# Kernel optimization log

Hardware: AMD Instinct MI355X
Metric: run time of the kernel (lower is better)

## Reference

```python
import jax, jax.numpy as jnp
import numpy as np

B_IMG, T_PER, DIN = 8, 4096, 1176
D, E, BN, L, TOP_K, OUT = 1024, 8, 64, 4, 2, 4096


def setup_inputs() -> dict:
    key = jax.random.key(0)
    ks = jax.random.split(key, 16)
    s = 0.02
    inp = {
        "pixel_values": jax.random.normal(ks[0], (B_IMG * T_PER, DIN), jnp.float32),
        "image_grid_thw": jnp.tile(jnp.array([[1, 64, 64]], dtype=jnp.int64), (B_IMG, 1)),
        # in_proj (no bias)
        "w_in": jax.random.normal(ks[1], (DIN, D), jnp.float32) * s,
        # skin classifier: Linear(D,64) -> ReLU -> Linear(64,3)
        "w_sc1": jax.random.normal(ks[2], (D, 64), jnp.float32) * s,
        "b_sc1": jnp.zeros((64,), jnp.float32),
        "w_sc2": jax.random.normal(ks[3], (64, 3), jnp.float32) * s,
        "b_sc2": jnp.zeros((3,), jnp.float32),
        # per-adapter-layer routers (stacked over L)
        "w_rimg": jax.random.normal(ks[4], (L, D, E), jnp.float32) * s,
        "w_rskin": jax.random.normal(ks[5], (L, 3, E), jnp.float32) * s,
        # per-layer, per-expert MLP: Linear(D,BN) -> ReLU -> Linear(BN,D)
        "ew1": jax.random.normal(ks[6], (L, E, D, BN), jnp.float32) * s,
        "eb1": jnp.zeros((L, E, BN), jnp.float32),
        "ew2": jax.random.normal(ks[7], (L, E, BN, D), jnp.float32) * s,
        "eb2": jnp.zeros((L, E, D), jnp.float32),
        # out_proj
        "w_out": jax.random.normal(ks[8], (D, OUT), jnp.float32) * s,
        "b_out": jnp.zeros((OUT,), jnp.float32),
    }
    return inp


def _forward(pixel_values, image_grid_thw, w_in, w_sc1, b_sc1, w_sc2, b_sc2,
             w_rimg, w_rskin, ew1, eb1, ew2, eb2, w_out, b_out):
    B = image_grid_thw.shape[0]
    T = pixel_values.shape[0] // B  # equal chunk sizes (t*h*w identical per image)
    x = pixel_values.reshape(B, T, -1)

    def per_image(xc):  # xc: [T, din]
        h = xc @ w_in  # [T, D]
        g = h.mean(0)
        skin_logits = jax.nn.relu(g @ w_sc1 + b_sc1) @ w_sc2 + b_sc2  # [3]
        skin_probs = jax.nn.softmax(skin_logits)

        def layer(carry, params):
            h, aux = carry
            wri, wrs, W1, B1, W2, B2 = params
            logits = h @ wri + skin_probs @ wrs  # [T, E]
            probs = jax.nn.softmax(logits, axis=-1)
            tp, ti = jax.lax.top_k(probs, TOP_K)
            tp = tp / (tp.sum(-1, keepdims=True) + 1e-6)
            rows = jnp.arange(h.shape[0])[:, None]
            # dense per-token expert weights (0 for non-selected experts)
            wfull = jnp.zeros_like(probs).at[rows, ti].add(tp)
            mask = jnp.zeros_like(probs).at[rows, ti].add(1.0)
            h1 = jax.nn.relu(jnp.einsum('td,edb->teb', h, W1) + B1)  # [T,E,BN]
            h2 = jnp.einsum('teb,ebd->ted', h1, W2) + B2             # [T,E,D]
            moe_out = jnp.einsum('ted,te->td', h2, wfull)
            aux = aux + (probs.mean(0) * mask.mean(0)).sum() * probs.shape[-1]
            return (h + moe_out, aux), None

        (h, aux), _ = jax.lax.scan(layer, (h, jnp.zeros((), h.dtype)),
                                   (w_rimg, w_rskin, ew1, eb1, ew2, eb2))
        return h.mean(0), skin_logits, aux

    pooled, skin_logits, aux = jax.vmap(per_image)(x)
    vision_proj = pooled @ w_out + b_out
    return pooled, vision_proj, aux.sum(), skin_logits


def reference(pixel_values, image_grid_thw, w_in, w_sc1, b_sc1, w_sc2, b_sc2,
              w_rimg, w_rskin, ew1, eb1, ew2, eb2, w_out, b_out):
    return _forward(pixel_values, image_grid_thw, w_in, w_sc1, b_sc1, w_sc2, b_sc2,
                    w_rimg, w_rskin, ew1, eb1, ew2, eb2, w_out, b_out)
```

## Files before the change

kernel.cpp:

```cpp
#include <hip/hip_runtime.h>
#include <math.h>

#define TPI  4096
#define TT   32768
#define DIN  1176
#define KP   1184
#define DM   1024
#define NE   8
#define BN   64
#define NL   4
#define DOUT 4096

typedef __attribute__((ext_vector_type(4))) float floatx4;
typedef __attribute__((ext_vector_type(8))) short bf16x8;
typedef unsigned int uint;

__device__ inline short f2bf(float x) {
    unsigned u = __float_as_uint(x);
    u += 0x7fffu + ((u >> 16) & 1u);
    return (short)(u >> 16);
}
__device__ inline float bf2f(short h) {
    return __uint_as_float(((unsigned)(unsigned short)h) << 16);
}

#define GLP(p) ((const __attribute__((address_space(1))) void*)(p))
#define LDSP(p) ((__attribute__((address_space(3))) void*)(p))
#define ASYNC16(g, s) __builtin_amdgcn_global_load_lds(GLP(g), LDSP(s), 16, 0, 0)

#define OFF_H0    0ul
#define OFF_H1    67108864ul
#define OFF_XB    134217728ul
#define OFF_WBT   211812352ul
#define OFF_E1T   214237184ul
#define OFF_E2T   218431488ul
#define OFF_BTOK  222625792ul
#define OFF_BW1   222756864ul
#define OFF_BW2   222887936ul
#define OFF_T2E   223019008ul
#define OFF_T2W   223150080ul
#define OFF_WQ    223412224ul
#define OFF_Z     223416320ul
#define Z_BYTES   39232ul
#define OFF_RB    223455552ul
#define OFF_WRT   223456576ul

__global__ __launch_bounds__(256) void convx_kernel(
    const float* __restrict__ X, short* __restrict__ Xb)
{
    const long row = blockIdx.x;
    const float* src = X + row * (long)DIN;
    short* dst = Xb + row * (long)KP;
    for (int i = threadIdx.x; i < 296; i += 256) {
        short4 s;
        if (i < 294) {
            float4 v = *(const float4*)(src + i * 4);
            s.x = f2bf(v.x); s.y = f2bf(v.y); s.z = f2bf(v.z); s.w = f2bf(v.w);
        } else {
            s.x = 0; s.y = 0; s.z = 0; s.w = 0;
        }
        *(short4*)(dst + i * 4) = s;
    }
}

__global__ __launch_bounds__(256) void transp_kernel(
    const float* __restrict__ src, short* __restrict__ dst, int RS, int CS, int DK)
{
    __shared__ float tb[64][65];
    const int kt = blockIdx.x * 64, nt = blockIdx.y * 64;
    const long sb = (long)blockIdx.z * RS * CS;
    const long db = (long)blockIdx.z * CS * DK;
    const int rr = threadIdx.x >> 6, cc = threadIdx.x & 63;
#pragma unroll
    for (int i = 0; i < 16; ++i) {
        int r = i * 4 + rr;
        int k = kt + r, n = nt + cc;
        tb[r][cc] = (k < RS && n < CS) ? src[sb + (long)k * CS + n] : 0.0f;
    }
    __syncthreads();
#pragma unroll
    for (int i = 0; i < 16; ++i) {
        int r = i * 4 + rr;
        int n = nt + r, k = kt + cc;
        if (n < CS && k < DK) dst[db + (long)n * DK + k] = f2bf(tb[cc][r]);
    }
}

__global__ __launch_bounds__(256) void wrt_kernel(
    const float* __restrict__ w_rimg, short* __restrict__ wrT)
{
    const int l = blockIdx.x >> 4, e = blockIdx.x & 15;
    short* dst = wrT + ((long)l * 16 + e) * 1024;
    if (e < 8) {
        const float* src = w_rimg + (long)l * 8192 + e;
        for (int k = threadIdx.x; k < 1024; k += 256) dst[k] = f2bf(src[k * 8]);
    } else {
        for (int k = threadIdx.x; k < 1024; k += 256) dst[k] = 0;
    }
}

__global__ __launch_bounds__(256) void gemm_in_mfma(
    const short* __restrict__ Xb, const short* __restrict__ Wbt, short* __restrict__ Hb)
{
    __shared__ __align__(16) short As[128 * 32];
    __shared__ __align__(16) short Bs[128 * 32];
    const int tid = threadIdx.x;
    const int m0 = blockIdx.x * 128, n0 = blockIdx.y * 128;
    const int w = tid >> 6, lane = tid & 63;
    const int quad = lane >> 4, l15 = lane & 15;
    const int wm = (w >> 1) * 64, wn = (w & 1) * 64;

    floatx4 acc[4][4];
#pragma unroll
    for (int i = 0; i < 4; ++i)
#pragma unroll
        for (int j = 0; j < 4; ++j) acc[i][j] = 0.0f;

    const int r0 = tid >> 2, kof = (tid & 3) * 8;
    const int r1 = (tid + 256) >> 2;
    const short* a0p = Xb + (long)(m0 + r0) * KP + kof;
    const short* a1p = Xb + (long)(m0 + r1) * KP + kof;
    const short* b0p = Wbt + (long)(n0 + r0) * KP + kof;
    const short* b1p = Wbt + (long)(n0 + r1) * KP + kof;
    short* as0 = As + tid * 8;
    short* as1 = As + (tid + 256) * 8;
    short* bs0 = Bs + tid * 8;
    short* bs1 = Bs + (tid + 256) * 8;

    for (int k0 = 0; k0 < KP; k0 += 32) {
        __syncthreads();
        ASYNC16(a0p + k0, as0);
        ASYNC16(a1p + k0, as1);
        ASYNC16(b0p + k0, bs0);
        ASYNC16(b1p + k0, bs1);
        __syncthreads();
        bf16x8 af[4], bfr[4];
#pragma unroll
        for (int i = 0; i < 4; ++i)
            af[i] = *(const bf16x8*)&As[(wm + i * 16 + l15) * 32 + quad * 8];
#pragma unroll
        for (int j = 0; j < 4; ++j)
            bfr[j] = *(const bf16x8*)&Bs[(wn + j * 16 + l15) * 32 + quad * 8];
#pragma unroll
        for (int i = 0; i < 4; ++i)
#pragma unroll
            for (int j = 0; j < 4; ++j)
                acc[i][j] = __builtin_amdgcn_mfma_f32_16x16x32_bf16(af[i], bfr[j], acc[i][j], 0, 0, 0);
    }
#pragma unroll
    for (int i = 0; i < 4; ++i)
#pragma unroll
        for (int j = 0; j < 4; ++j)
#pragma unroll
            for (int r = 0; r < 4; ++r)
                Hb[(long)(m0 + wm + i * 16 + quad * 4 + r) * DM + n0 + wn + j * 16 + l15] =
                    f2bf(acc[i][j][r]);
}

__global__ __launch_bounds__(256) void colmean_kernel(
    const short* __restrict__ Hb, float* __restrict__ outp)
{
    const int col = blockIdx.x * 256 + threadIdx.x;
    const int img = blockIdx.y;
    const int t0 = blockIdx.z * 256;
    const short* p = Hb + ((long)img * TPI + t0) * DM + col;
    float s = 0.0f;
#pragma unroll 8
    for (int t = 0; t < 256; ++t) s += bf2f(p[(long)t * DM]);
    atomicAdd(&outp[img * DM + col], s * (1.0f / 4096.0f));
}

__global__ __launch_bounds__(256) void skin1_kernel(
    const float* __restrict__ g, const float* __restrict__ w_sc1,
    const float* __restrict__ b_sc1, float* __restrict__ hsg)
{
    __shared__ float red[4][64];
    const int img = blockIdx.x;
    const int part = threadIdx.x >> 6, c = threadIdx.x & 63;
    float s = 0.0f;
    for (int i = 0; i < 256; ++i) {
        int d = part * 256 + i;
        s += g[img * DM + d] * w_sc1[d * 64 + c];
    }
    red[part][c] = s;
    __syncthreads();
    if (part == 0) {
        float v = red[0][c] + red[1][c] + red[2][c] + red[3][c] + b_sc1[c];
        hsg[img * 64 + c] = fmaxf(v, 0.0f);
    }
}

__global__ __launch_bounds__(256) void skin2_kernel(
    const float* __restrict__ hsg, const float* __restrict__ w_sc2, const float* __restrict__ b_sc2,
    const float* __restrict__ w_rskin, float* __restrict__ skin_logits_out, float* __restrict__ rb)
{
    __shared__ float l3[24];
    __shared__ float sp[24];
    const int tid = threadIdx.x;
    if (tid < 24) {
        int img = tid / 3, j = tid % 3;
        float s = b_sc2[j];
        for (int c = 0; c < 64; ++c) s += hsg[img * 64 + c] * w_sc2[c * 3 + j];
        l3[tid] = s;
        skin_logits_out[tid] = s;
    }
    __syncthreads();
    if (tid < 8) {
        float v0 = l3[tid * 3], v1 = l3[tid * 3 + 1], v2 = l3[tid * 3 + 2];
        float m = fmaxf(v0, fmaxf(v1, v2));
        float e0 = expf(v0 - m), e1 = expf(v1 - m), e2 = expf(v2 - m);
        float inv = 1.0f / (e0 + e1 + e2);
        sp[tid * 3] = e0 * inv; sp[tid * 3 + 1] = e1 * inv; sp[tid * 3 + 2] = e2 * inv;
    }
    __syncthreads();
    {
        int l = tid >> 6, img = (tid >> 3) & 7, e = tid & 7;
        float s = 0.0f;
#pragma unroll
        for (int c = 0; c < 3; ++c) s += sp[img * 3 + c] * w_rskin[(l * 3 + c) * 8 + e];
        rb[tid] = s;
    }
}

__global__ __launch_bounds__(256) void router_kernel(
    const short* __restrict__ Hb, const short* __restrict__ wrT, const float* __restrict__ rb,
    uint* __restrict__ top2e, float* __restrict__ top2w, int* __restrict__ counts_pair,
    float* __restrict__ sum_probs, float* __restrict__ mask_cnt, int l)
{
    __shared__ __align__(16) short As[8 * 64 * 32];
    __shared__ float lgS[64 * 9];
    const int tid = threadIdx.x;
    const int tok0 = blockIdx.x * 64;
    const int img = tok0 >> 12;
    const int w = tid >> 6, lane = tid & 63;
    const int quad = lane >> 4, l15 = lane & 15;

    const short* rowptr = Hb + (long)(tok0 + w * 16 + (lane >> 2)) * DM + (lane & 3) * 8;
    short* sdst = As + tid * 8;
    const short* wrl = wrT + (long)l * 16 * 1024 + l15 * 1024 + quad * 8;

    floatx4 acc = 0.0f;
    for (int k0 = 0; k0 < DM; k0 += 256) {
        __syncthreads();
#pragma unroll
        for (int c = 0; c < 8; ++c) ASYNC16(rowptr + k0 + c * 32, sdst + c * 2048);
        __syncthreads();
#pragma unroll
        for (int c = 0; c < 8; ++c) {
            bf16x8 af = *(const bf16x8*)&As[c * 2048 + (w * 16 + l15) * 32 + quad * 8];
            bf16x8 bf = *(const bf16x8*)(wrl + k0 + c * 32);
            acc = __builtin_amdgcn_mfma_f32_16x16x32_bf16(af, bf, acc, 0, 0, 0);
        }
    }
    if (l15 < 8) {
#pragma unroll
        for (int r = 0; r < 4; ++r) lgS[(w * 16 + quad * 4 + r) * 9 + l15] = acc[r];
    }
    __syncthreads();

    if (tid < 64) {
        const int token = tok0 + tid;
        float p[8];
        float mx = -1e30f;
#pragma unroll
        for (int e = 0; e < 8; ++e) {
            float v = lgS[tid * 9 + e] + rb[l * 64 + img * 8 + e];
            p[e] = v; mx = fmaxf(mx, v);
        }
        float s = 0.0f;
#pragma unroll
        for (int e = 0; e < 8; ++e) { p[e] = expf(p[e] - mx); s += p[e]; }
        float inv = 1.0f / s;
#pragma unroll
        for (int e = 0; e < 8; ++e) p[e] *= inv;

        int i1 = 0; float b1v = p[0];
#pragma unroll
        for (int e = 1; e < 8; ++e) if (p[e] > b1v) { b1v = p[e]; i1 = e; }
        int i2 = -1; float b2v = -1.0f;
#pragma unroll
        for (int e = 0; e < 8; ++e) if (e != i1 && p[e] > b2v) { b2v = p[e]; i2 = e; }
        float den = b1v + b2v + 1e-6f;
        top2e[token] = (uint)i1 | ((uint)i2 << 8);
        top2w[2 * token] = b1v / den;
        top2w[2 * token + 1] = b2v / den;

        atomicAdd(&counts_pair[l * 64 + i1 * 8 + i2], 1);

        for (int slot = 0; slot < 2; ++slot) {
            int esel = slot ? i2 : i1;
#pragma unroll
            for (int e = 0; e < 8; ++e) {
                unsigned long long m = __ballot(esel == e);
                int pc = __popcll(m);
                if (pc && tid == (__ffsll(m) - 1))
                    atomicAdd(&mask_cnt[l * 64 + img * 8 + e], (float)pc);
            }
        }
#pragma unroll
        for (int e = 0; e < 8; ++e) {
            float r = p[e];
            for (int off = 32; off > 0; off >>= 1) r += __shfl_down(r, off);
            if (tid == 0) atomicAdd(&sum_probs[l * 64 + img * 8 + e], r);
        }
    }
}

__global__ __launch_bounds__(64) void wq_kernel(
    const int* __restrict__ counts_pair, int* __restrict__ wq, int* __restrict__ nworkp,
    int* __restrict__ pair_off, int l)
{
    const int p = threadIdx.x;
    int cnt = counts_pair[l * 64 + p];
    int x = cnt;
    for (int off = 1; off < 64; off <<= 1) {
        int y = __shfl_up(x, off);
        if (p >= off) x += y;
    }
    pair_off[p] = x - cnt;
    int nb = (cnt + 63) >> 6;
    int t = nb;
    for (int off = 1; off < 64; off <<= 1) {
        int y = __shfl_up(t, off);
        if (p >= off) t += y;
    }
    int start = t - nb;
    for (int i = 0; i < nb; ++i) wq[start + i] = p | ((i * 64) << 6);
    if (p == 63) nworkp[0] = t;
}

__global__ __launch_bounds__(256) void scatter_kernel(
    const uint* __restrict__ top2e, const float* __restrict__ top2w,
    const int* __restrict__ pair_off, int* __restrict__ cursors,
    int* __restrict__ btok, float* __restrict__ bw1, float* __restrict__ bw2, int l)
{
    const int t = blockIdx.x * 256 + threadIdx.x;
    const int lane = threadIdx.x & 63;
    uint pe = top2e[t];
    int p = (int)(pe & 255u) * 8 + (int)((pe >> 8) & 255u);
    float w1 = top2w[2 * t], w2 = top2w[2 * t + 1];
    int myoff = pair_off[p];
    unsigned long long rem = __ballot(true);
    while (rem) {
        int leader = __ffsll(rem) - 1;
        int pv = __shfl(p, leader);
        unsigned long long m = __ballot(p == pv);
        int basep = 0;
        if (lane == leader) basep = atomicAdd(&cursors[l * 64 + pv], __popcll(m));
        basep = __shfl(basep, leader);
        if (p == pv) {
            int pos = basep + __popcll(m & ((1ull << lane) - 1ull));
            int s = myoff + pos;
            btok[s] = t;
            bw1[s] = w1;
            bw2[s] = w2;
        }
        rem &= ~m;
    }
}

__global__ __launch_bounds__(256) void expert_pair(
    const short* __restrict__ Hin, short* __restrict__ Hout,
    const int* __restrict__ counts_pair, const int* __restrict__ pair_off,
    const int* __restrict__ btok, const float* __restrict__ bw1, const float* __restrict__ bw2,
    const short* __restrict__ ew1t, const float* __restrict__ eb1,
    const short* __restrict__ ew2t, const float* __restrict__ eb2,
    const int* __restrict__ wq, const int* __restrict__ nworkp, int l)
{
    __shared__ __align__(16) short As[8 * 64 * 32];
    __shared__ __align__(16) short h1a[64 * 72];
    __shared__ __align__(16) short h1b[64 * 72];
    __shared__ int tkS[64];
    __shared__ float w1S[64], w2S[64];

    const int tid = threadIdx.x;
    const int w = tid >> 6, lane = tid & 63;
    const int quad = lane >> 4, l15 = lane & 15;
    const int nwork = nworkp[0];
    short* sdst = As + tid * 8;

    for (int wi = blockIdx.x; wi < nwork; wi += gridDim.x) {
        const int item = wq[wi];
        const int p = item & 63, base = item >> 6;
        const int ea = p >> 3, eb = p & 7;
        const int off = pair_off[p];
        const int cnt = counts_pair[l * 64 + p];

        __syncthreads();
        if (tid < 64) {
            bool valid = (base + tid) < cnt;
            int s = off + base + tid;
            tkS[tid] = valid ? btok[s] : 0;
            w1S[tid] = valid ? bw1[s] : 0.0f;
            w2S[tid] = valid ? bw2[s] : 0.0f;
        }
        __syncthreads();
        const int lea = l * 8 + ea, leb = l * 8 + eb;
        const short* rowptr = Hin + (long)tkS[w * 16 + (lane >> 2)] * DM + (lane & 3) * 8;

        floatx4 acc1a[4], acc1b[4];
#pragma unroll
        for (int i = 0; i < 4; ++i) { acc1a[i] = 0.0f; acc1b[i] = 0.0f; }
        const short* w1ap = ew1t + ((long)lea * 64 + w * 16 + l15) * DM + quad * 8;
        const short* w1bp = ew1t + ((long)leb * 64 + w * 16 + l15) * DM + quad * 8;

        for (int k0 = 0; k0 < DM; k0 += 256) {
            __syncthreads();
#pragma unroll
            for (int c = 0; c < 8; ++c) ASYNC16(rowptr + k0 + c * 32, sdst + c * 2048);
            __syncthreads();
#pragma unroll
            for (int c = 0; c < 8; ++c) {
                bf16x8 ba = *(const bf16x8*)(w1ap + k0 + c * 32);
                bf16x8 bb = *(const bf16x8*)(w1bp + k0 + c * 32);
#pragma unroll
                for (int i = 0; i < 4; ++i) {
                    bf16x8 af = *(const bf16x8*)&As[c * 2048 + (i * 16 + l15) * 32 + quad * 8];
                    acc1a[i] = __builtin_amdgcn_mfma_f32_16x16x32_bf16(af, ba, acc1a[i], 0, 0, 0);
                    acc1b[i] = __builtin_amdgcn_mfma_f32_16x16x32_bf16(af, bb, acc1b[i], 0, 0, 0);
                }
            }
        }
        {
            float b1av = eb1[lea * BN + w * 16 + l15];
            float b1bv = eb1[leb * BN + w * 16 + l15];
#pragma unroll
            for (int i = 0; i < 4; ++i)
#pragma unroll
                for (int r = 0; r < 4; ++r) {
                    h1a[(i * 16 + quad * 4 + r) * 72 + w * 16 + l15] =
                        f2bf(fmaxf(acc1a[i][r] + b1av, 0.0f));
                    h1b[(i * 16 + quad * 4 + r) * 72 + w * 16 + l15] =
                        f2bf(fmaxf(acc1b[i][r] + b1bv, 0.0f));
                }
        }
        __syncthreads();

        const short* w2ap = ew2t + ((long)lea * DM + w * 16 + l15) * 64 + quad * 8;
        const short* w2bp = ew2t + ((long)leb * DM + w * 16 + l15) * 64 + quad * 8;
        const bool rowvalid = (base + (tid >> 2)) < cnt;
        const long orow = (long)tkS[tid >> 2] * DM;

        for (int gidx = 0; gidx < 4; ++gidx) {
            const int g0 = gidx * 256;
#pragma unroll
            for (int c = 0; c < 8; ++c) ASYNC16(rowptr + g0 + c * 32, sdst + c * 2048);
            __syncthreads();
#pragma unroll
            for (int ns = 0; ns < 4; ++ns) {
                const int n0 = g0 + ns * 64;
                floatx4 a2a[4], a2b[4];
#pragma unroll
                for (int tj = 0; tj < 4; ++tj) { a2a[tj] = 0.0f; a2b[tj] = 0.0f; }
#pragma unroll
                for (int kk = 0; kk < 2; ++kk) {
                    bf16x8 wa = *(const bf16x8*)(w2ap + (long)n0 * 64 + kk * 32);
                    bf16x8 wb = *(const bf16x8*)(w2bp + (long)n0 * 64 + kk * 32);
#pragma unroll
                    for (int tj = 0; tj < 4; ++tj) {
                        bf16x8 ha = *(const bf16x8*)&h1a[(tj * 16 + l15) * 72 + kk * 32 + quad * 8];
                        bf16x8 hb = *(const bf16x8*)&h1b[(tj * 16 + l15) * 72 + kk * 32 + quad * 8];
                        a2a[tj] = __builtin_amdgcn_mfma_f32_16x16x32_bf16(wa, ha, a2a[tj], 0, 0, 0);
                        a2b[tj] = __builtin_amdgcn_mfma_f32_16x16x32_bf16(wb, hb, a2b[tj], 0, 0, 0);
                    }
                }
                const int nloc = ns * 64 + w * 16 + quad * 4;
                const int csub = nloc >> 5, cidx = nloc & 31;
                float4 b2av = *(const float4*)&eb2[lea * DM + g0 + nloc];
                float4 b2bv = *(const float4*)&eb2[leb * DM + g0 + nloc];
#pragma unroll
                for (int tj = 0; tj < 4; ++tj) {
                    int tk = tj * 16 + l15;
                    float w1 = w1S[tk], w2 = w2S[tk];
                    short* slot = &As[csub * 2048 + tk * 32 + cidx];
                    short4 res = *(short4*)slot;
                    short4 o;
                    o.x = f2bf(bf2f(res.x) + w1 * (a2a[tj][0] + b2av.x) + w2 * (a2b[tj][0] + b2bv.x));
                    o.y = f2bf(bf2f(res.y) + w1 * (a2a[tj][1] + b2av.y) + w2 * (a2b[tj][1] + b2bv.y));
                    o.z = f2bf(bf2f(res.z) + w1 * (a2a[tj][2] + b2av.z) + w2 * (a2b[tj][2] + b2bv.z));
                    o.w = f2bf(bf2f(res.w) + w1 * (a2a[tj][3] + b2av.w) + w2 * (a2b[tj][3] + b2bv.w));
                    *(short4*)slot = o;
                }
            }
            __syncthreads();
            if (rowvalid) {
                const int tok = tid >> 2;
#pragma unroll
                for (int c2 = 0; c2 < 2; ++c2) {
                    const int csub = (tid & 3) * 2 + c2;
#pragma unroll
                    for (int j = 0; j < 4; ++j) {
                        int4 v = *(const int4*)&As[csub * 2048 + tok * 32 + j * 8];
                        *(int4*)(Hout + orow + g0 + csub * 32 + j * 8) = v;
                    }
                }
            }
            __syncthreads();
        }
    }
}

__global__ __launch_bounds__(256) void vproj_kernel(
    const float* __restrict__ pooled, const float* __restrict__ w_out,
    const float* __restrict__ b_out, float* __restrict__ outp)
{
    __shared__ float ps[8 * 128];
    const int tid = threadIdx.x;
    const int n = blockIdx.x * 256 + tid;
    const int d0 = blockIdx.y * 128;
#pragma unroll
    for (int i = 0; i < 4; ++i) {
        int idx = tid + i * 256;
        ps[idx] = pooled[(idx >> 7) * DM + d0 + (idx & 127)];
    }
    __syncthreads();
    float acc[8];
    float binit = (blockIdx.y == 0) ? b_out[n] : 0.0f;
#pragma unroll
    for (int img = 0; img < 8; ++img) acc[img] = binit;
    for (int d = 0; d < 128; ++d) {
        float wv = w_out[(long)(d0 + d) * DOUT + n];
#pragma unroll
        for (int img = 0; img < 8; ++img) acc[img] += ps[img * 128 + d] * wv;
    }
#pragma unroll
    for (int img = 0; img < 8; ++img) atomicAdd(&outp[img * DOUT + n], acc[img]);
}

__global__ __launch_bounds__(64) void aux_kernel(
    const float* __restrict__ sum_probs, const float* __restrict__ mask_cnt,
    float* __restrict__ outp)
{
    const int tid = threadIdx.x;
    float v = 0.0f;
    if (tid < 32) {
        float s = 0.0f;
#pragma unroll
        for (int e = 0; e < 8; ++e) s += sum_probs[tid * 8 + e] * mask_cnt[tid * 8 + e];
        v = s * (8.0f / (4096.0f * 4096.0f));
    }
    for (int off = 32; off > 0; off >>= 1) v += __shfl_down(v, off);
    if (tid == 0) outp[0] = v;
}

extern "C" void kernel_launch(void* const* d_in, const int* in_sizes, int n_in,
                              void* d_out, int out_size, void* d_ws, size_t ws_size,
                              hipStream_t stream) {
    const float* X       = (const float*)d_in[0];
    const float* w_in    = (const float*)d_in[2];
    const float* w_sc1   = (const float*)d_in[3];
    const float* b_sc1   = (const float*)d_in[4];
    const float* w_sc2   = (const float*)d_in[5];
    const float* b_sc2   = (const float*)d_in[6];
    const float* w_rimg  = (const float*)d_in[7];
    const float* w_rskin = (const float*)d_in[8];
    const float* ew1     = (const float*)d_in[9];
    const float* eb1     = (const float*)d_in[10];
    const float* ew2     = (const float*)d_in[11];
    const float* eb2     = (const float*)d_in[12];
    const float* w_out   = (const float*)d_in[13];
    const float* b_out   = (const float*)d_in[14];

    float* out = (float*)d_out;
    char* ws = (char*)d_ws;

    short* H0   = (short*)(ws + OFF_H0);
    short* H1   = (short*)(ws + OFF_H1);
    short* Xb   = (short*)(ws + OFF_XB);
    short* Wbt  = (short*)(ws + OFF_WBT);
    short* ew1t = (short*)(ws + OFF_E1T);
    short* ew2t = (short*)(ws + OFF_E2T);
    int*   btok = (int*)(ws + OFF_BTOK);
    float* bw1  = (float*)(ws + OFF_BW1);
    float* bw2  = (float*)(ws + OFF_BW2);
    uint*  top2e = (uint*)(ws + OFF_T2E);
    float* top2w = (float*)(ws + OFF_T2W);
    int*   wq    = (int*)(ws + OFF_WQ);
    int*   counts_pair = (int*)(ws + OFF_Z);
    int*   cursors     = (int*)(ws + OFF_Z + 1024);
    int*   nworkp      = (int*)(ws + OFF_Z + 2048);
    int*   pair_off    = (int*)(ws + OFF_Z + 2112);
    float* sum_probs   = (float*)(ws + OFF_Z + 2368);
    float* mask_cnt    = (float*)(ws + OFF_Z + 3392);
    float* g           = (float*)(ws + OFF_Z + 4416);
    float* hsg         = (float*)(ws + OFF_Z + 37184);
    float* rb          = (float*)(ws + OFF_RB);
    short* wrT         = (short*)(ws + OFF_WRT);

    hipMemsetAsync(d_out, 0, (size_t)out_size * sizeof(float), stream);
    hipMemsetAsync(ws + OFF_Z, 0, Z_BYTES, stream);

    dim3 b256(256);
    convx_kernel<<<TT, b256, 0, stream>>>(X, Xb);
    transp_kernel<<<dim3(19, 16, 1), b256, 0, stream>>>(w_in, Wbt, DIN, DM, KP);
    transp_kernel<<<dim3(16, 1, 32), b256, 0, stream>>>(ew1, ew1t, DM, BN, DM);
    transp_kernel<<<dim3(1, 16, 32), b256, 0, stream>>>(ew2, ew2t, BN, DM, BN);
    wrt_kernel<<<64, b256, 0, stream>>>(w_rimg, wrT);
    gemm_in_mfma<<<dim3(256, 8), b256, 0, stream>>>(Xb, Wbt, H0);
    colmean_kernel<<<dim3(4, 8, 16), b256, 0, stream>>>(H0, g);
    skin1_kernel<<<8, b256, 0, stream>>>(g, w_sc1, b_sc1, hsg);
    skin2_kernel<<<1, b256, 0, stream>>>(hsg, w_sc2, b_sc2, w_rskin, out + 40961, rb);

    short* Hc = H0;
    short* Hn = H1;
    for (int l = 0; l < NL; ++l) {
        router_kernel<<<512, b256, 0, stream>>>(Hc, wrT, rb, top2e, top2w,
                                                counts_pair, sum_probs, mask_cnt, l);
        wq_kernel<<<1, 64, 0, stream>>>(counts_pair, wq, nworkp, pair_off, l);
        scatter_kernel<<<128, b256, 0, stream>>>(top2e, top2w, pair_off, cursors,
                                                 btok, bw1, bw2, l);
        expert_pair<<<576, b256, 0, stream>>>(Hc, Hn, counts_pair, pair_off, btok, bw1, bw2,
                                              ew1t, eb1, ew2t, eb2, wq, nworkp, l);
        short* tmp = Hc; Hc = Hn; Hn = tmp;
    }
    colmean_kernel<<<dim3(4, 8, 16), b256, 0, stream>>>(Hc, out);
    vproj_kernel<<<dim3(16, 8), b256, 0, stream>>>(out, w_out, b_out, out + 8192);
    aux_kernel<<<1, 64, 0, stream>>>(sum_probs, mask_cnt, out + 40960);
}
```

Before: 1.493 ms.

## Fuse routing scatter into router and switch expert kernel to per-wave 16-token tiles

The router now computes softmax and top-2 with wave shuffles straight from MFMA accumulators and writes each token into a fixed-capacity per-pair bin via an atomic. This removes the separate scatter kernel and the prefix-offset pass. The expert kernel now has each wave handle its own 16-token item and read activations and weights directly from global memory instead of staging 64-token tiles in LDS with block barriers. This cuts synchronisation and launch count, but loses the LDS reuse of weights across 64 tokens and makes the output stores uncoalesced and scattered, and bin order is now nondeterministic.

```diff
diff --git a/kernel.cpp b/kernel.cpp
--- a/kernel.cpp
+++ b/kernel.cpp
@@ -10,6 +10,7 @@
 #define BN   64
 #define NL   4
 #define DOUT 4096
+#define BINCAP 32768
 
 typedef __attribute__((ext_vector_type(4))) float floatx4;
 typedef __attribute__((ext_vector_type(8))) short bf16x8;
@@ -35,15 +36,13 @@
 #define OFF_E1T   214237184ul
 #define OFF_E2T   218431488ul
 #define OFF_BTOK  222625792ul
-#define OFF_BW1   222756864ul
-#define OFF_BW2   222887936ul
-#define OFF_T2E   223019008ul
-#define OFF_T2W   223150080ul
-#define OFF_WQ    223412224ul
-#define OFF_Z     223416320ul
-#define Z_BYTES   39232ul
-#define OFF_RB    223455552ul
-#define OFF_WRT   223456576ul
+#define OFF_BW1   231014400ul
+#define OFF_BW2   239403008ul
+#define OFF_WQ    247791616ul
+#define OFF_Z     247808000ul
+#define Z_BYTES   37952ul
+#define OFF_RB    247845952ul
+#define OFF_WRT   247846976ul
 
 __global__ __launch_bounds__(256) void convx_kernel(
     const float* __restrict__ X, short* __restrict__ Xb)
@@ -224,278 +223,193 @@
 
 __global__ __launch_bounds__(256) void router_kernel(
     const short* __restrict__ Hb, const short* __restrict__ wrT, const float* __restrict__ rb,
-    uint* __restrict__ top2e, float* __restrict__ top2w, int* __restrict__ counts_pair,
+    int* __restrict__ counts, int* __restrict__ btok, float* __restrict__ bw1, float* __restrict__ bw2,
     float* __restrict__ sum_probs, float* __restrict__ mask_cnt, int l)
 {
-    __shared__ __align__(16) short As[8 * 64 * 32];
-    __shared__ float lgS[64 * 9];
     const int tid = threadIdx.x;
-    const int tok0 = blockIdx.x * 64;
-    const int img = tok0 >> 12;
     const int w = tid >> 6, lane = tid & 63;
     const int quad = lane >> 4, l15 = lane & 15;
-
-    const short* rowptr = Hb + (long)(tok0 + w * 16 + (lane >> 2)) * DM + (lane & 3) * 8;
-    short* sdst = As + tid * 8;
-    const short* wrl = wrT + (long)l * 16 * 1024 + l15 * 1024 + quad * 8;
+    const int tok0w = blockIdx.x * 64 + w * 16;
+    const int img = tok0w >> 12;
+
+    const short* arow = Hb + (long)(tok0w + l15) * DM + quad * 8;
+    const short* brow = wrT + ((long)l * 16 + l15) * 1024 + quad * 8;
 
     floatx4 acc = 0.0f;
-    for (int k0 = 0; k0 < DM; k0 += 256) {
-        __syncthreads();
-#pragma unroll
-        for (int c = 0; c < 8; ++c) ASYNC16(rowptr + k0 + c * 32, sdst + c * 2048);
-        __syncthreads();
-#pragma unroll
-        for (int c = 0; c < 8; ++c) {
-            bf16x8 af = *(const bf16x8*)&As[c * 2048 + (w * 16 + l15) * 32 + quad * 8];
-            bf16x8 bf = *(const bf16x8*)(wrl + k0 + c * 32);
-            acc = __builtin_amdgcn_mfma_f32_16x16x32_bf16(af, bf, acc, 0, 0, 0);
-        }
-    }
-    if (l15 < 8) {
-#pragma unroll
-        for (int r = 0; r < 4; ++r) lgS[(w * 16 + quad * 4 + r) * 9 + l15] = acc[r];
-    }
-    __syncthreads();
-
-    if (tid < 64) {
-        const int token = tok0 + tid;
-        float p[8];
-        float mx = -1e30f;
-#pragma unroll
-        for (int e = 0; e < 8; ++e) {
-            float v = lgS[tid * 9 + e] + rb[l * 64 + img * 8 + e];
-            p[e] = v; mx = fmaxf(mx, v);
-        }
-        float s = 0.0f;
-#pragma unroll
-        for (int e = 0; e < 8; ++e) { p[e] = expf(p[e] - mx); s += p[e]; }
-        float inv = 1.0f / s;
-#pragma unroll
-        for (int e = 0; e < 8; ++e) p[e] *= inv;
-
-        int i1 = 0; float b1v = p[0];
-#pragma unroll
-        for (int e = 1; e < 8; ++e) if (p[e] > b1v) { b1v = p[e]; i1 = e; }
-        int i2 = -1; float b2v = -1.0f;
-#pragma unroll
-        for (int e = 0; e < 8; ++e) if (e != i1 && p[e] > b2v) { b2v = p[e]; i2 = e; }
-        float den = b1v + b2v + 1e-6f;
-        top2e[token] = (uint)i1 | ((uint)i2 << 8);
-        top2w[2 * token] = b1v / den;
-        top2w[2 * token + 1] = b2v / den;
-
-        atomicAdd(&counts_pair[l * 64 + i1 * 8 + i2], 1);
-
-        for (int slot = 0; slot < 2; ++slot) {
-            int esel = slot ? i2 : i1;
-#pragma unroll
-            for (int e = 0; e < 8; ++e) {
-                unsigned long long m = __ballot(esel == e);
-                int pc = __popcll(m);
-                if (pc && tid == (__ffsll(m) - 1))
-                    atomicAdd(&mask_cnt[l * 64 + img * 8 + e], (float)pc);
-            }
-        }
-#pragma unroll
-        for (int e = 0; e < 8; ++e) {
-            float r = p[e];
-            for (int off = 32; off > 0; off >>= 1) r += __shfl_down(r, off);
-            if (tid == 0) atomicAdd(&sum_probs[l * 64 + img * 8 + e], r);
+#pragma unroll 8
+    for (int k0 = 0; k0 < DM; k0 += 32) {
+        bf16x8 a = *(const bf16x8*)(arow + k0);
+        bf16x8 b = *(const bf16x8*)(brow + k0);
+        acc = __builtin_amdgcn_mfma_f32_16x16x32_bf16(a, b, acc, 0, 0, 0);
+    }
+
+    const float rbv = rb[l * 64 + img * 8 + (l15 & 7)];
+    float pr[4]; int i1r[4], i2r[4]; float w1r[4], w2r[4];
+#pragma unroll
+    for (int r = 0; r < 4; ++r) {
+        float v = (l15 < 8) ? (acc[r] + rbv) : -3.0e38f;
+        float mx = v;
+#pragma unroll
+        for (int m = 1; m < 16; m <<= 1) mx = fmaxf(mx, __shfl_xor(mx, m));
+        float ex = (l15 < 8) ? expf(v - mx) : 0.0f;
+        float s = ex;
+#pragma unroll
+        for (int m = 1; m < 16; m <<= 1) s += __shfl_xor(s, m);
+        float p = ex / s;
+        pr[r] = p;
+        float tv = p; int ti = l15;
+#pragma unroll
+        for (int m = 1; m < 16; m <<= 1) {
+            float ov = __shfl_xor(tv, m); int oi = __shfl_xor(ti, m);
+            if (ov > tv || (ov == tv && oi < ti)) { tv = ov; ti = oi; }
+        }
+        int i1 = ti; float p1 = tv;
+        float tv2 = (l15 == i1) ? -1.0f : p; int ti2 = l15;
+#pragma unroll
+        for (int m = 1; m < 16; m <<= 1) {
+            float ov = __shfl_xor(tv2, m); int oi = __shfl_xor(ti2, m);
+            if (ov > tv2 || (ov == tv2 && oi < ti2)) { tv2 = ov; ti2 = oi; }
+        }
+        int i2 = ti2; float p2 = tv2;
+        float den = p1 + p2 + 1e-6f;
+        i1r[r] = i1; i2r[r] = i2; w1r[r] = p1 / den; w2r[r] = p2 / den;
+    }
+
+    float ps = pr[0] + pr[1] + pr[2] + pr[3];
+    ps += __shfl_xor(ps, 16); ps += __shfl_xor(ps, 32);
+    float mc = 0.0f;
+#pragma unroll
+    for (int r = 0; r < 4; ++r) mc += (i1r[r] == l15 ? 1.0f : 0.0f) + (i2r[r] == l15 ? 1.0f : 0.0f);
+    mc += __shfl_xor(mc, 16); mc += __shfl_xor(mc, 32);
+    if (lane < 8) {
+        atomicAdd(&sum_probs[l * 64 + img * 8 + lane], ps);
+        atomicAdd(&mask_cnt[l * 64 + img * 8 + lane], mc);
+    }
+    if (l15 == 0) {
+#pragma unroll
+        for (int r = 0; r < 4; ++r) {
+            int token = tok0w + quad * 4 + r;
+            int p = i1r[r] * 8 + i2r[r];
+            int pos = atomicAdd(&counts[l * 64 + p], 1);
+            int sidx = p * BINCAP + pos;
+            btok[sidx] = token;
+            bw1[sidx] = w1r[r];
+            bw2[sidx] = w2r[r];
         }
     }
 }
 
 __global__ __launch_bounds__(64) void wq_kernel(
-    const int* __restrict__ counts_pair, int* __restrict__ wq, int* __restrict__ nworkp,
-    int* __restrict__ pair_off, int l)
+    const int* __restrict__ counts, int* __restrict__ wq, int* __restrict__ nworkp, int l)
 {
     const int p = threadIdx.x;
-    int cnt = counts_pair[l * 64 + p];
-    int x = cnt;
-    for (int off = 1; off < 64; off <<= 1) {
-        int y = __shfl_up(x, off);
-        if (p >= off) x += y;
-    }
-    pair_off[p] = x - cnt;
-    int nb = (cnt + 63) >> 6;
+    int cnt = counts[l * 64 + p];
+    int nb = (cnt + 15) >> 4;
     int t = nb;
     for (int off = 1; off < 64; off <<= 1) {
         int y = __shfl_up(t, off);
         if (p >= off) t += y;
     }
     int start = t - nb;
-    for (int i = 0; i < nb; ++i) wq[start + i] = p | ((i * 64) << 6);
+    for (int i = 0; i < nb; ++i) wq[start + i] = p | ((i * 16) << 6);
     if (p == 63) nworkp[0] = t;
-}
-
-__global__ __launch_bounds__(256) void scatter_kernel(
-    const uint* __restrict__ top2e, const float* __restrict__ top2w,
-    const int* __restrict__ pair_off, int* __restrict__ cursors,
-    int* __restrict__ btok, float* __restrict__ bw1, float* __restrict__ bw2, int l)
-{
-    const int t = blockIdx.x * 256 + threadIdx.x;
-    const int lane = threadIdx.x & 63;
-    uint pe = top2e[t];
-    int p = (int)(pe & 255u) * 8 + (int)((pe >> 8) & 255u);
-    float w1 = top2w[2 * t], w2 = top2w[2 * t + 1];
-    int myoff = pair_off[p];
-    unsigned long long rem = __ballot(true);
-    while (rem) {
-        int leader = __ffsll(rem) - 1;
-        int pv = __shfl(p, leader);
-        unsigned long long m = __ballot(p == pv);
-        int basep = 0;
-        if (lane == leader) basep = atomicAdd(&cursors[l * 64 + pv], __popcll(m));
-        basep = __shfl(basep, leader);
-        if (p == pv) {
-            int pos = basep + __popcll(m & ((1ull << lane) - 1ull));
-            int s = myoff + pos;
-            btok[s] = t;
-            bw1[s] = w1;
-            bw2[s] = w2;
-        }
-        rem &= ~m;
-    }
 }
 
 __global__ __launch_bounds__(256) void expert_pair(
     const short* __restrict__ Hin, short* __restrict__ Hout,
-    const int* __restrict__ counts_pair, const int* __restrict__ pair_off,
-    const int* __restrict__ btok, const float* __restrict__ bw1, const float* __restrict__ bw2,
+    const int* __restrict__ counts, const int* __restrict__ btok,
+    const float* __restrict__ bw1, const float* __restrict__ bw2,
     const short* __restrict__ ew1t, const float* __restrict__ eb1,
     const short* __restrict__ ew2t, const float* __restrict__ eb2,
     const int* __restrict__ wq, const int* __restrict__ nworkp, int l)
 {
-    __shared__ __align__(16) short As[8 * 64 * 32];
-    __shared__ __align__(16) short h1a[64 * 72];
-    __shared__ __align__(16) short h1b[64 * 72];
-    __shared__ int tkS[64];
-    __shared__ float w1S[64], w2S[64];
-
+    __shared__ __align__(16) short h1sh[4][2][16 * 72];
     const int tid = threadIdx.x;
     const int w = tid >> 6, lane = tid & 63;
     const int quad = lane >> 4, l15 = lane & 15;
     const int nwork = nworkp[0];
-    short* sdst = As + tid * 8;
-
-    for (int wi = blockIdx.x; wi < nwork; wi += gridDim.x) {
+    short* ha_sh = &h1sh[w][0][0];
+    short* hb_sh = &h1sh[w][1][0];
+
+    for (int wi = blockIdx.x * 4 + w; wi < nwork; wi += gridDim.x * 4) {
         const int item = wq[wi];
-        const int p = item & 63, base = item >> 6;
+        const int p = item & 63;
+        const int base = item >> 6;
         const int ea = p >> 3, eb = p & 7;
-        const int off = pair_off[p];
-        const int cnt = counts_pair[l * 64 + p];
-
-        __syncthreads();
-        if (tid < 64) {
-            bool valid = (base + tid) < cnt;
-            int s = off + base + tid;
-            tkS[tid] = valid ? btok[s] : 0;
-            w1S[tid] = valid ? bw1[s] : 0.0f;
-            w2S[tid] = valid ? bw2[s] : 0.0f;
-        }
-        __syncthreads();
         const int lea = l * 8 + ea, leb = l * 8 + eb;
-        const short* rowptr = Hin + (long)tkS[w * 16 + (lane >> 2)] * DM + (lane & 3) * 8;
+        const int cnt = counts[l * 64 + p];
+
+        const int sidx = p * BINCAP + base + l15;
+        const bool vmeta = (base + l15) < cnt;
+        const int mytok = vmeta ? btok[sidx] : 0;
+        const float myw1 = vmeta ? bw1[sidx] : 0.0f;
+        const float myw2 = vmeta ? bw2[sidx] : 0.0f;
+
+        const short* arow = Hin + (long)mytok * DM + quad * 8;
+        const short* w1a = ew1t + ((long)lea * 64 + l15) * DM + quad * 8;
+        const short* w1b = ew1t + ((long)leb * 64 + l15) * DM + quad * 8;
 
         floatx4 acc1a[4], acc1b[4];
 #pragma unroll
         for (int i = 0; i < 4; ++i) { acc1a[i] = 0.0f; acc1b[i] = 0.0f; }
-        const short* w1ap = ew1t + ((long)lea * 64 + w * 16 + l15) * DM + quad * 8;
-        const short* w1bp = ew1t + ((long)leb * 64 + w * 16 + l15) * DM + quad * 8;
-
-        for (int k0 = 0; k0 < DM; k0 += 256) {
-            __syncthreads();
-#pragma unroll
-            for (int c = 0; c < 8; ++c) ASYNC16(rowptr + k0 + c * 32, sdst + c * 2048);
-            __syncthreads();
-#pragma unroll
-            for (int c = 0; c < 8; ++c) {
-                bf16x8 ba = *(const bf16x8*)(w1ap + k0 + c * 32);
-                bf16x8 bb = *(const bf16x8*)(w1bp + k0 + c * 32);
-#pragma unroll
-                for (int i = 0; i < 4; ++i) {
-                    bf16x8 af = *(const bf16x8*)&As[c * 2048 + (i * 16 + l15) * 32 + quad * 8];
-                    acc1a[i] = __builtin_amdgcn_mfma_f32_16x16x32_bf16(af, ba, acc1a[i], 0, 0, 0);
-                    acc1b[i] = __builtin_amdgcn_mfma_f32_16x16x32_bf16(af, bb, acc1b[i], 0, 0, 0);
+
+        for (int k0 = 0; k0 < DM; k0 += 32) {
+            bf16x8 a = *(const bf16x8*)(arow + k0);
+#pragma unroll
+            for (int bt = 0; bt < 4; ++bt) {
+                bf16x8 ba = *(const bf16x8*)(w1a + (long)bt * 16 * DM + k0);
+                bf16x8 bb = *(const bf16x8*)(w1b + (long)bt * 16 * DM + k0);
+                acc1a[bt] = __builtin_amdgcn_mfma_f32_16x16x32_bf16(a, ba, acc1a[bt], 0, 0, 0);
+                acc1b[bt] = __builtin_amdgcn_mfma_f32_16x16x32_bf16(a, bb, acc1b[bt], 0, 0, 0);
+            }
+        }
+#pragma unroll
+        for (int bt = 0; bt < 4; ++bt) {
+            float b1a = eb1[lea * BN + bt * 16 + l15];
+            float b1b = eb1[leb * BN + bt * 16 + l15];
+#pragma unroll
+            for (int r = 0; r < 4; ++r) {
+                ha_sh[(quad * 4 + r) * 72 + bt * 16 + l15] = f2bf(fmaxf(acc1a[bt][r] + b1a, 0.0f));
+                hb_sh[(quad * 4 + r) * 72 + bt * 16 + l15] = f2bf(fmaxf(acc1b[bt][r] + b1b, 0.0f));
+            }
+        }
+        bf16x8 ha0 = *(const bf16x8*)&ha_sh[l15 * 72 + quad * 8];
+        bf16x8 ha1 = *(const bf16x8*)&ha_sh[l15 * 72 + 32 + quad * 8];
+        bf16x8 hb0 = *(const bf16x8*)&hb_sh[l15 * 72 + quad * 8];
+        bf16x8 hb1 = *(const bf16x8*)&hb_sh[l15 * 72 + 32 + quad * 8];
+
+        int tokr[4]; float w1rr[4], w2rr[4]; bool vr[4];
+#pragma unroll
+        for (int r = 0; r < 4; ++r) {
+            tokr[r] = __shfl(mytok, quad * 4 + r);
+            w1rr[r] = __shfl(myw1, quad * 4 + r);
+            w2rr[r] = __shfl(myw2, quad * 4 + r);
+            vr[r] = (base + quad * 4 + r) < cnt;
+        }
+
+        const short* w2a = ew2t + ((long)lea * DM + l15) * 64 + quad * 8;
+        const short* w2b = ew2t + ((long)leb * DM + l15) * 64 + quad * 8;
+        for (int n0 = 0; n0 < DM; n0 += 16) {
+            const long wo = (long)n0 * 64;
+            bf16x8 wa0 = *(const bf16x8*)(w2a + wo);
+            bf16x8 wa1 = *(const bf16x8*)(w2a + wo + 32);
+            bf16x8 wb0 = *(const bf16x8*)(w2b + wo);
+            bf16x8 wb1 = *(const bf16x8*)(w2b + wo + 32);
+            floatx4 a2 = 0.0f, b2 = 0.0f;
+            a2 = __builtin_amdgcn_mfma_f32_16x16x32_bf16(ha0, wa0, a2, 0, 0, 0);
+            a2 = __builtin_amdgcn_mfma_f32_16x16x32_bf16(ha1, wa1, a2, 0, 0, 0);
+            b2 = __builtin_amdgcn_mfma_f32_16x16x32_bf16(hb0, wb0, b2, 0, 0, 0);
+            b2 = __builtin_amdgcn_mfma_f32_16x16x32_bf16(hb1, wb1, b2, 0, 0, 0);
+            float bba = eb2[lea * DM + n0 + l15];
+            float bbb = eb2[leb * DM + n0 + l15];
+#pragma unroll
+            for (int r = 0; r < 4; ++r) {
+                if (vr[r]) {
+                    long idx = (long)tokr[r] * DM + n0 + l15;
+                    float res = bf2f(Hin[idx]);
+                    Hout[idx] = f2bf(res + w1rr[r] * (a2[r] + bba) + w2rr[r] * (b2[r] + bbb));
                 }
             }
-        }
-        {
-            float b1av = eb1[lea * BN + w * 16 + l15];
-            float b1bv = eb1[leb * BN + w * 16 + l15];
-#pragma unroll
-            for (int i = 0; i < 4; ++i)
-#pragma unroll
-                for (int r = 0; r < 4; ++r) {
-                    h1a[(i * 16 + quad * 4 + r) * 72 + w * 16 + l15] =
-                        f2bf(fmaxf(acc1a[i][r] + b1av, 0.0f));
-                    h1b[(i * 16 + quad * 4 + r) * 72 + w * 16 + l15] =
-                        f2bf(fmaxf(acc1b[i][r] + b1bv, 0.0f));
-                }
-        }
-        __syncthreads();
-
-        const short* w2ap = ew2t + ((long)lea * DM + w * 16 + l15) * 64 + quad * 8;
-        const short* w2bp = ew2t + ((long)leb * DM + w * 16 + l15) * 64 + quad * 8;
-        const bool rowvalid = (base + (tid >> 2)) < cnt;
-        const long orow = (long)tkS[tid >> 2] * DM;
-
-        for (int gidx = 0; gidx < 4; ++gidx) {
-            const int g0 = gidx * 256;
-#pragma unroll
-            for (int c = 0; c < 8; ++c) ASYNC16(rowptr + g0 + c * 32, sdst + c * 2048);
-            __syncthreads();
-#pragma unroll
-            for (int ns = 0; ns < 4; ++ns) {
-                const int n0 = g0 + ns * 64;
-                floatx4 a2a[4], a2b[4];
-#pragma unroll
-                for (int tj = 0; tj < 4; ++tj) { a2a[tj] = 0.0f; a2b[tj] = 0.0f; }
-#pragma unroll
-                for (int kk = 0; kk < 2; ++kk) {
-                    bf16x8 wa = *(const bf16x8*)(w2ap + (long)n0 * 64 + kk * 32);
-                    bf16x8 wb = *(const bf16x8*)(w2bp + (long)n0 * 64 + kk * 32);
-#pragma unroll
-                    for (int tj = 0; tj < 4; ++tj) {
-                        bf16x8 ha = *(const bf16x8*)&h1a[(tj * 16 + l15) * 72 + kk * 32 + quad * 8];
-                        bf16x8 hb = *(const bf16x8*)&h1b[(tj * 16 + l15) * 72 + kk * 32 + quad * 8];
-                        a2a[tj] = __builtin_amdgcn_mfma_f32_16x16x32_bf16(wa, ha, a2a[tj], 0, 0, 0);
-                        a2b[tj] = __builtin_amdgcn_mfma_f32_16x16x32_bf16(wb, hb, a2b[tj], 0, 0, 0);
-                    }
-                }
-                const int nloc = ns * 64 + w * 16 + quad * 4;
-                const int csub = nloc >> 5, cidx = nloc & 31;
-                float4 b2av = *(const float4*)&eb2[lea * DM + g0 + nloc];
-                float4 b2bv = *(const float4*)&eb2[leb * DM + g0 + nloc];
-#pragma unroll
-                for (int tj = 0; tj < 4; ++tj) {
-                    int tk = tj * 16 + l15;
-                    float w1 = w1S[tk], w2 = w2S[tk];
-                    short* slot = &As[csub * 2048 + tk * 32 + cidx];
-                    short4 res = *(short4*)slot;
-                    short4 o;
-                    o.x = f2bf(bf2f(res.x) + w1 * (a2a[tj][0] + b2av.x) + w2 * (a2b[tj][0] + b2bv.x));
-                    o.y = f2bf(bf2f(res.y) + w1 * (a2a[tj][1] + b2av.y) + w2 * (a2b[tj][1] + b2bv.y));
-                    o.z = f2bf(bf2f(res.z) + w1 * (a2a[tj][2] + b2av.z) + w2 * (a2b[tj][2] + b2bv.z));
-                    o.w = f2bf(bf2f(res.w) + w1 * (a2a[tj][3] + b2av.w) + w2 * (a2b[tj][3] + b2bv.w));
-                    *(short4*)slot = o;
-                }
-            }
-            __syncthreads();
-            if (rowvalid) {
-                const int tok = tid >> 2;
-#pragma unroll
-                for (int c2 = 0; c2 < 2; ++c2) {
-                    const int csub = (tid & 3) * 2 + c2;
-#pragma unroll
-                    for (int j = 0; j < 4; ++j) {
-                        int4 v = *(const int4*)&As[csub * 2048 + tok * 32 + j * 8];
-                        *(int4*)(Hout + orow + g0 + csub * 32 + j * 8) = v;
-                    }
-                }
-            }
-            __syncthreads();
         }
     }
 }
@@ -573,19 +487,15 @@
     int*   btok = (int*)(ws + OFF_BTOK);
     float* bw1  = (float*)(ws + OFF_BW1);
     float* bw2  = (float*)(ws + OFF_BW2);
-    uint*  top2e = (uint*)(ws + OFF_T2E);
-    float* top2w = (float*)(ws + OFF_T2W);
-    int*   wq    = (int*)(ws + OFF_WQ);
-    int*   counts_pair = (int*)(ws + OFF_Z);
-    int*   cursors     = (int*)(ws + OFF_Z + 1024);
-    int*   nworkp      = (int*)(ws + OFF_Z + 2048);
-    int*   pair_off    = (int*)(ws + OFF_Z + 2112);
-    float* sum_probs   = (float*)(ws + OFF_Z + 2368);
-    float* mask_cnt    = (float*)(ws + OFF_Z + 3392);
-    float* g           = (float*)(ws + OFF_Z + 4416);
-    float* hsg         = (float*)(ws + OFF_Z + 37184);
-    float* rb          = (float*)(ws + OFF_RB);
-    short* wrT         = (short*)(ws + OFF_WRT);
+    int*   wq   = (int*)(ws + OFF_WQ);
+    int*   counts    = (int*)(ws + OFF_Z);
+    int*   nworkp    = (int*)(ws + OFF_Z + 1024);
+    float* sum_probs = (float*)(ws + OFF_Z + 1088);
+    float* mask_cnt  = (float*)(ws + OFF_Z + 2112);
+    float* g         = (float*)(ws + OFF_Z + 3136);
+    float* hsg       = (float*)(ws + OFF_Z + 35904);
+    float* rb        = (float*)(ws + OFF_RB);
+    short* wrT       = (short*)(ws + OFF_WRT);
 
     hipMemsetAsync(d_out, 0, (size_t)out_size * sizeof(float), stream);
     hipMemsetAsync(ws + OFF_Z, 0, Z_BYTES, stream);
@@ -604,12 +514,10 @@
     short* Hc = H0;
     short* Hn = H1;
     for (int l = 0; l < NL; ++l) {
-        router_kernel<<<512, b256, 0, stream>>>(Hc, wrT, rb, top2e, top2w,
-                                                counts_pair, sum_probs, mask_cnt, l);
-        wq_kernel<<<1, 64, 0, stream>>>(counts_pair, wq, nworkp, pair_off, l);
-        scatter_kernel<<<128, b256, 0, stream>>>(top2e, top2w, pair_off, cursors,
-                                                 btok, bw1, bw2, l);
-        expert_pair<<<576, b256, 0, stream>>>(Hc, Hn, counts_pair, pair_off, btok, bw1, bw2,
+        router_kernel<<<512, b256, 0, stream>>>(Hc, wrT, rb, counts, btok, bw1, bw2,
+                                                sum_probs, mask_cnt, l);
+        wq_kernel<<<1, 64, 0, stream>>>(counts, wq, nworkp, l);
+        expert_pair<<<640, b256, 0, stream>>>(Hc, Hn, counts, btok, bw1, bw2,
                                               ew1t, eb1, ew2t, eb2, wq, nworkp, l);
         short* tmp = Hc; Hc = Hn; Hn = tmp;
     }
```

After: 1.934 ms. 1.3x slower.
